# Performance work log

Measured on AMD Instinct MI355X. Metric: run time of the kernel, lower is better.

Reference implementation:

```python
import jax, jax.numpy as jnp
import numpy as np

D_MODEL = 1024
D_STATE = 128
D_CONV = 4
EXPAND = 2
HEADDIM = 64
D_INNER = EXPAND * D_MODEL            # 2048
NHEADS = D_INNER // HEADDIM           # 32
D_IN_PROJ = 2 * D_INNER + 2 * D_STATE + NHEADS  # z, xBC, dt
CONV_DIM = D_INNER + 2 * D_STATE      # depthwise-conv channels


def setup_inputs() -> dict:
    key = jax.random.key(0)
    ks = jax.random.split(key, 8)
    B, L = 2, 2048
    s = lambda k, shape, sc=0.02: jax.random.normal(k, shape, jnp.float32) * sc
    return dict(
        x=jax.random.normal(ks[0], (B, L, D_MODEL), jnp.float32),
        norm1_w=jnp.ones((D_MODEL,), jnp.float32),
        in_proj_w=s(ks[1], (D_IN_PROJ, D_MODEL)),
        conv_w=s(ks[2], (CONV_DIM, D_CONV), 0.2),
        conv_b=jnp.zeros((CONV_DIM,), jnp.float32),
        dt_bias=jnp.log(jnp.expm1(jax.random.uniform(ks[3], (NHEADS,), jnp.float32, 0.001, 0.1))),
        A_log=jnp.log(jax.random.uniform(ks[4], (NHEADS,), jnp.float32, 1.0, 16.0)),
        D=jnp.ones((NHEADS,), jnp.float32),
        mnorm_w=jnp.ones((D_INNER,), jnp.float32),
        out_proj_w=s(ks[5], (D_MODEL, D_INNER)),
        norm2_w=jnp.ones((D_MODEL,), jnp.float32),
        mlp_w1=s(ks[6], (4 * D_MODEL, D_MODEL)),
        mlp_b1=jnp.zeros((4 * D_MODEL,), jnp.float32),
        mlp_w2=s(ks[7], (D_MODEL, 4 * D_MODEL)),
        mlp_b2=jnp.zeros((D_MODEL,), jnp.float32),
    )


def _block_norm(x, w, eps=1e-6):
    # Faithful to source: rms = sqrt(||x||_2^2 + eps) (their .mean(-1) is over a size-1 dim)
    return w * x / jnp.sqrt(jnp.sum(x * x, axis=-1, keepdims=True) + eps)


def _mamba2(x, in_proj_w, conv_w, conv_b, dt_bias, A_log, D, mnorm_w, out_proj_w):
    b, l, _ = x.shape
    zxbcdt = x @ in_proj_w.T                                   # (b,l,D_IN_PROJ)
    z, xBC, dt_raw = jnp.split(zxbcdt, [D_INNER, D_INNER + CONV_DIM], axis=-1)
    # causal depthwise conv1d + silu over (x,B,C)
    pad = jnp.pad(xBC, ((0, 0), (D_CONV - 1, 0), (0, 0)))
    conv = sum(pad[:, k:k + l, :] * conv_w[None, None, :, k] for k in range(D_CONV)) + conv_b
    xBC = jax.nn.silu(conv)
    xh, Bm, Cm = jnp.split(xBC, [D_INNER, D_INNER + D_STATE], axis=-1)
    xh = xh.reshape(b, l, NHEADS, HEADDIM)
    dt = jax.nn.softplus(dt_raw + dt_bias)                     # (b,l,h)
    A = -jnp.exp(A_log)                                        # (h,) scalar-A per head

    def step(hs, inp):
        x_t, dt_t, B_t, C_t = inp                              # (b,h,p),(b,h),(b,n),(b,n)
        dA = jnp.exp(dt_t * A)[:, :, None, None]               # (b,h,1,1)
        hs = hs * dA + (dt_t[:, :, None] * x_t)[..., None] * B_t[:, None, None, :]
        y_t = jnp.einsum('bhpn,bn->bhp', hs, C_t)
        return hs, y_t

    hs0 = jnp.zeros((b, NHEADS, HEADDIM, D_STATE), x.dtype)
    _, ys = jax.lax.scan(step, hs0, (xh.transpose(1, 0, 2, 3), dt.transpose(1, 0, 2),
                                     Bm.transpose(1, 0, 2), Cm.transpose(1, 0, 2)))
    y = ys.transpose(1, 0, 2, 3) + D[None, None, :, None] * xh  # D skip
    y = y.reshape(b, l, D_INNER)
    y = y * jax.nn.silu(z)                                      # gated RMSNorm (mamba2 default)
    y = y / jnp.sqrt(jnp.mean(y * y, axis=-1, keepdims=True) + 1e-5) * mnorm_w
    return y @ out_proj_w.T


def reference(x, norm1_w, in_proj_w, conv_w, conv_b, dt_bias, A_log, D, mnorm_w,
              out_proj_w, norm2_w, mlp_w1, mlp_b1, mlp_w2, mlp_b2):
    x = x + _mamba2(_block_norm(x, norm1_w), in_proj_w, conv_w, conv_b,
                    dt_bias, A_log, D, mnorm_w, out_proj_w)
    h = _block_norm(x, norm2_w)
    h = jax.nn.gelu(h @ mlp_w1.T + mlp_b1, approximate=False) @ mlp_w2.T + mlp_b2
    return x + h
```

## Files before the change

### kernel.cpp

```cpp
#include <hip/hip_runtime.h>
#include <hip/hip_bf16.h>
#include <cstdint>

#define L_SEQ   2048
#define BATCH   2
#define ROWS    (BATCH*L_SEQ)
#define DMODEL  1024
#define DINNER  2048
#define DSTATE  128
#define NHEADS  32
#define DIN_PROJ 4384
#define DIN_PAD  4480
#define CONVDIM  2304
#define DMLP    4096
#define CHUNK   64
#define NCHUNK  (L_SEQ/CHUNK)

typedef __attribute__((ext_vector_type(4))) float f32x4;
typedef __attribute__((ext_vector_type(8))) short bf16x8;
typedef __attribute__((ext_vector_type(4))) short bf16x4;
typedef __attribute__((ext_vector_type(2))) short bf16x2;

static __device__ __forceinline__ short f2bf(float f) {
  union { float f; unsigned int i; } v; v.f = f;
  unsigned int r = v.i + 0x7fffu + ((v.i >> 16) & 1u);
  return (short)(r >> 16);
}
static __device__ __forceinline__ float bf2f(short s) {
  union { unsigned int i; float f; } v; v.i = ((unsigned int)(unsigned short)s) << 16;
  return v.f;
}

static __device__ __forceinline__ void gl2lds16(const void* g, void* l) {
  __builtin_amdgcn_global_load_lds((const __attribute__((address_space(1))) void*)g,
                                   (__attribute__((address_space(3))) void*)l, 16, 0, 0);
}

__global__ __launch_bounds__(256) void cvt_kernel(const float* __restrict__ src, short* __restrict__ dst,
                                                  long rows_src, int kshift)
{
  long i = (((long)blockIdx.x) * 256 + threadIdx.x) * 4;
  long r = i >> kshift;
  bf16x4 o;
  if (r < rows_src) {
    f32x4 v = *(const f32x4*)&src[i];
    o[0] = f2bf(v[0]); o[1] = f2bf(v[1]); o[2] = f2bf(v[2]); o[3] = f2bf(v[3]);
  } else {
    o[0] = 0; o[1] = 0; o[2] = 0; o[3] = 0;
  }
  *(bf16x4*)&dst[i] = o;
}

__global__ __launch_bounds__(256) void rmsnorm_l2_kernel(const float* __restrict__ in,
                                                         const float* __restrict__ w,
                                                         short* __restrict__ out)
{
  int row = blockIdx.x, tid = threadIdx.x;
  const float* xr = in + (long)row * DMODEL;
  f32x4 v = *(const f32x4*)&xr[tid * 4];
  float s = v[0]*v[0] + v[1]*v[1] + v[2]*v[2] + v[3]*v[3];
  for (int o = 32; o; o >>= 1) s += __shfl_down(s, o);
  __shared__ float red[4];
  if ((tid & 63) == 0) red[tid >> 6] = s;
  __syncthreads();
  float sc = rsqrtf(red[0] + red[1] + red[2] + red[3] + 1e-6f);
  f32x4 wv = *(const f32x4*)&w[tid * 4];
  bf16x4 o;
  #pragma unroll
  for (int j = 0; j < 4; j++) o[j] = f2bf(v[j] * sc * wv[j]);
  *(bf16x4*)&out[(long)row * DMODEL + tid * 4] = o;
}

template<int EPI, int STG>
__global__ __launch_bounds__(256)
void gemm_bt_kernel(const short* __restrict__ A, const short* __restrict__ W,
                    const float* __restrict__ bias, const float* __restrict__ resid,
                    void* __restrict__ out, int N, int K)
{
  __shared__ short As[STG][128*64];
  __shared__ short Ws[STG][128*64];
  const int tid = threadIdx.x;
  const int lane = tid & 63, wid = tid >> 6;
  const int wm = wid >> 1, wn = wid & 1;
  const long arow0 = (long)blockIdx.x * 128;
  const long wrow0 = (long)blockIdx.y * 128;
  const int srow = tid >> 3;
  const int sslot = (tid & 7) ^ (srow & 7);
  const int sdst = (tid >> 3) * 64 + (tid & 7) * 8;

  f32x4 acc[4][4];
  #pragma unroll
  for (int m = 0; m < 4; m++)
    #pragma unroll
    for (int n = 0; n < 4; n++)
      #pragma unroll
      for (int j = 0; j < 4; j++) acc[m][n][j] = 0.f;

  auto stage = [&](int buf, long kt) {
    #pragma unroll
    for (int i = 0; i < 4; i++)
      gl2lds16(A + (arow0 + i*32 + srow) * (long)K + kt + sslot*8, &As[buf][i*2048 + sdst]);
    #pragma unroll
    for (int i = 0; i < 4; i++)
      gl2lds16(W + (wrow0 + i*32 + srow) * (long)K + kt + sslot*8, &Ws[buf][i*2048 + sdst]);
  };

  const int nt = K >> 6;
  #pragma unroll
  for (int s = 0; s < STG - 1; s++) stage(s, s << 6);

  const int swz = (lane & 7) << 3;
  for (int t = 0; t < nt; t++) {
    if (t + STG - 1 < nt) {
      stage((t + STG - 1) & (STG - 1), (long)(t + STG - 1) << 6);
      asm volatile("s_waitcnt vmcnt(8)"  ::: "memory");
    } else {
      asm volatile("s_waitcnt vmcnt(0)" ::: "memory");
    }
    __builtin_amdgcn_s_barrier();
    __builtin_amdgcn_sched_barrier(0);
    const int cur = t & (STG - 1);
    #pragma unroll
    for (int kk = 0; kk < 64; kk += 32) {
      bf16x8 a[4], b[4];
      const int ko = kk + (lane >> 4) * 8;
      #pragma unroll
      for (int m = 0; m < 4; m++) {
        int row = wm*64 + m*16 + (lane & 15);
        a[m] = *(const bf16x8*)&As[cur][(row*64 + ko) ^ swz];
      }
      #pragma unroll
      for (int n = 0; n < 4; n++) {
        int row = wn*64 + n*16 + (lane & 15);
        b[n] = *(const bf16x8*)&Ws[cur][(row*64 + ko) ^ swz];
      }
      #pragma unroll
      for (int m = 0; m < 4; m++)
        #pragma unroll
        for (int n = 0; n < 4; n++)
          acc[m][n] = __builtin_amdgcn_mfma_f32_16x16x32_bf16(a[m], b[n], acc[m][n], 0, 0, 0);
    }
    asm volatile("s_waitcnt lgkmcnt(0)" ::: "memory");
    __builtin_amdgcn_sched_barrier(0);
    __builtin_amdgcn_s_barrier();
  }

  const int colf = lane & 15, rowf = (lane >> 4) * 4;
  #pragma unroll
  for (int m = 0; m < 4; m++)
    #pragma unroll
    for (int n = 0; n < 4; n++) {
      long col = wrow0 + wn*64 + n*16 + colf;
      #pragma unroll
      for (int j = 0; j < 4; j++) {
        long row = arow0 + wm*64 + m*16 + rowf + j;
        long idx = row * (long)N + col;
        ((short*)out)[idx] = f2bf(acc[m][n][j]);
      }
    }
}

template<int EPI>
__global__ __launch_bounds__(512)
void gemm256_kernel(const short* __restrict__ A, const short* __restrict__ W,
                    const float* __restrict__ bias, void* __restrict__ out, int N, int K)
{
  __shared__ short As[2][2][8192];
  __shared__ short Bs[2][2][8192];
  const int tid = threadIdx.x;
  const int lane = tid & 63, wid = tid >> 6;
  const int wm = wid >> 2, wn = wid & 3;
  const long arow0 = (long)blockIdx.x * 256;
  const long wrow0 = (long)blockIdx.y * 256;
  const int Kslice = K / gridDim.z;
  const long kbase = (long)blockIdx.z * Kslice;
  const int ntiles = Kslice >> 6;

  const int sr0 = tid >> 2, sr1 = sr0 + 128;
  const int ss  = tid & 3;
  const int scb0 = ss ^ ((sr0 >> 1) & 3);
  const int scb1 = ss ^ ((sr1 >> 1) & 3);
  const int sdst0 = tid * 8, sdst1 = tid * 8 + 4096;

  auto stageA = [&](int tau, int kh) {
    long colb = kbase + (long)tau * 64 + kh * 32;
    gl2lds16(A + (arow0 + sr0) * (long)K + colb + scb0 * 8, &As[tau & 1][kh][sdst0]);
    gl2lds16(A + (arow0 + sr1) * (long)K + colb + scb1 * 8, &As[tau & 1][kh][sdst1]);
  };
  auto stageB = [&](int tau, int kh) {
    long colb = kbase + (long)tau * 64 + kh * 32;
    gl2lds16(W + (wrow0 + sr0) * (long)K + colb + scb0 * 8, &Bs[tau & 1][kh][sdst0]);
    gl2lds16(W + (wrow0 + sr1) * (long)K + colb + scb1 * 8, &Bs[tau & 1][kh][sdst1]);
  };

  f32x4 acc[8][4];
  #pragma unroll
  for (int m = 0; m < 8; m++)
    #pragma unroll
    for (int n = 0; n < 4; n++)
      #pragma unroll
      for (int j = 0; j < 4; j++) acc[m][n][j] = 0.f;

  const int li = lane & 15;
  const int rcb = (((lane >> 4) ^ ((li >> 1) & 3))) * 8;

  stageA(0,0); stageB(0,0); stageA(0,1); stageB(0,1); stageA(1,0); stageB(1,0);
  asm volatile("s_waitcnt vmcnt(8)" ::: "memory");
  __builtin_amdgcn_s_barrier();

  bf16x8 a[8];
  auto phase = [&](int g, int kh, int nh) {
    const int buf = g & 1;
    if (nh == 0) {
      #pragma unroll
      for (int m = 0; m < 8; m++)
        a[m] = *(const bf16x8*)&As[buf][kh][(wm*128 + m*16 + li)*32 + rcb];
    }
    bf16x8 b0 = *(const bf16x8*)&Bs[buf][kh][(wn*64 + (nh*2    )*16 + li)*32 + rcb];
    bf16x8 b1 = *(const bf16x8*)&Bs[buf][kh][(wn*64 + (nh*2 + 1)*16 + li)*32 + rcb];
    if (kh == 0) {
      if (g + 1 < ntiles) { if (nh == 0) stageA(g+1, 1); else stageB(g+1, 1); }
    } else {
      if (g + 2 < ntiles) { if (nh == 0) stageA(g+2, 0); else stageB(g+2, 0); }
    }
    __builtin_amdgcn_s_barrier();
    asm volatile("s_waitcnt lgkmcnt(0)" ::: "memory");
    __builtin_amdgcn_sched_barrier(0);
    __builtin_amdgcn_s_setprio(1);
    #pragma unroll
    for (int m = 0; m < 8; m++) {
      acc[m][nh*2    ] = __builtin_amdgcn_mfma_f32_16x16x32_bf16(a[m], b0, acc[m][nh*2    ], 0, 0, 0);
      acc[m][nh*2 + 1] = __builtin_amdgcn_mfma_f32_16x16x32_bf16(a[m], b1, acc[m][nh*2 + 1], 0, 0, 0);
    }
    __builtin_amdgcn_s_setprio(0);
    if (kh == 0 && nh == 1) {
      if (g < ntiles - 1) asm volatile("s_waitcnt vmcnt(8)" ::: "memory");
      else                asm volatile("s_waitcnt vmcnt(0)" ::: "memory");
    } else if (kh == 1 && nh == 1 && g < ntiles - 1) {
      if (g < ntiles - 2) asm volatile("s_waitcnt vmcnt(8)" ::: "memory");
      else                asm volatile("s_waitcnt vmcnt(4)" ::: "memory");
    }
    __builtin_amdgcn_s_barrier();
  };

  for (int g = 0; g < ntiles; ++g) {
    phase(g, 0, 0); phase(g, 0, 1); phase(g, 1, 0); phase(g, 1, 1);
  }

  const int colf = lane & 15, rowf = (lane >> 4) * 4;
  const long MN = (long)gridDim.x * 256 * N;
  const long po = (long)blockIdx.z * MN;
  #pragma unroll
  for (int m = 0; m < 8; m++)
    #pragma unroll
    for (int n = 0; n < 4; n++) {
      long col = wrow0 + wn*64 + n*16 + colf;
      #pragma unroll
      for (int j = 0; j < 4; j++) {
        long row = arow0 + wm*128 + m*16 + rowf + j;
        long idx = row * (long)N + col;
        float v = acc[m][n][j];
        if (EPI == 2) {
          float t = v + bias[col];
          float ge = 0.5f * t * (1.f + erff(t * 0.70710678118654752f));
          ((short*)out)[idx] = f2bf(ge);
        } else {
          ((short*)out)[po + idx] = f2bf(v);
        }
      }
    }
}

template<bool BIAS>
__global__ __launch_bounds__(256) void reduce_split4_kernel(
    const short* __restrict__ part, const float* __restrict__ resid,
    const float* __restrict__ bias, float* __restrict__ out)
{
  long i = ((long)blockIdx.x * 256 + threadIdx.x) * 8;
  const long MN = (long)ROWS * DMODEL;
  bf16x8 p0 = *(const bf16x8*)&part[i];
  bf16x8 p1 = *(const bf16x8*)&part[i + MN];
  bf16x8 p2 = *(const bf16x8*)&part[i + 2*MN];
  bf16x8 p3 = *(const bf16x8*)&part[i + 3*MN];
  f32x4 r0 = *(const f32x4*)&resid[i];
  f32x4 r1 = *(const f32x4*)&resid[i + 4];
  f32x4 o0, o1;
  #pragma unroll
  for (int j = 0; j < 8; j++) {
    float s = (bf2f(p0[j]) + bf2f(p1[j])) + (bf2f(p2[j]) + bf2f(p3[j]));
    s += (j < 4) ? r0[j] : r1[j - 4];
    if (j < 4) o0[j] = s; else o1[j - 4] = s;
  }
  if (BIAS) {
    int c = (int)(i & (DMODEL - 1));
    f32x4 b0 = *(const f32x4*)&bias[c];
    f32x4 b1 = *(const f32x4*)&bias[c + 4];
    #pragma unroll
    for (int j = 0; j < 4; j++) { o0[j] += b0[j]; o1[j] += b1[j]; }
  }
  *(f32x4*)&out[i] = o0;
  *(f32x4*)&out[i + 4] = o1;
}

__global__ __launch_bounds__(256) void conv_dt_kernel(
    const short* __restrict__ zx, const float* __restrict__ cw, const float* __restrict__ cb,
    const float* __restrict__ dt_bias,
    short* __restrict__ xh, short* __restrict__ Bo, short* __restrict__ Co, float* __restrict__ dto)
{
  const int r0 = blockIdx.x * 8;
  const int tid = threadIdx.x;
  const bool interior = (r0 & (L_SEQ - 1)) != 0;

  auto conv8 = [&](int c0, auto&& emit) {
    const long col = DINNER + c0;
    f32x4 w[8]; float cbv[8];
    #pragma unroll
    for (int j = 0; j < 8; j++) { w[j] = *(const f32x4*)&cw[(c0 + j) * 4]; cbv[j] = cb[c0 + j]; }
    bf16x8 win[11];
    #pragma unroll
    for (int j = 0; j < 3; j++) {
      bf16x8 z;
      #pragma unroll
      for (int q = 0; q < 8; q++) z[q] = 0;
      win[j] = interior ? *(const bf16x8*)&zx[(long)(r0 - 3 + j) * DIN_PAD + col] : z;
    }
    #pragma unroll
    for (int j = 3; j < 11; j++)
      win[j] = *(const bf16x8*)&zx[(long)(r0 - 3 + j) * DIN_PAD + col];
    #pragma unroll
    for (int i = 0; i < 8; i++) {
      float a[8];
      #pragma unroll
      for (int j = 0; j < 8; j++) a[j] = cbv[j];
      #pragma unroll
      for (int k = 0; k < 4; k++)
        #pragma unroll
        for (int j = 0; j < 8; j++) a[j] = fmaf(bf2f(win[i + k][j]), w[j][k], a[j]);
      bf16x8 o;
      #pragma unroll
      for (int j = 0; j < 8; j++) { float s = a[j] / (1.f + __expf(-a[j])); o[j] = f2bf(s); }
      emit(i, o);
    }
  };

  {
    int c0 = tid * 8;
    conv8(c0, [&](int i, bf16x8 o) {
      *(bf16x8*)&xh[(long)(r0 + i) * DINNER + c0] = o;
    });
  }
  if (tid < 32) {
    int c0 = 2048 + tid * 8;
    conv8(c0, [&](int i, bf16x8 o) {
      if (c0 < 2048 + DSTATE) *(bf16x8*)&Bo[(long)(r0 + i) * DSTATE + (c0 - 2048)] = o;
      else                    *(bf16x8*)&Co[(long)(r0 + i) * DSTATE + (c0 - 2048 - DSTATE)] = o;
    });
  } else if (tid < 36) {
    int h0 = (tid - 32) * 8;
    float db[8];
    #pragma unroll
    for (int j = 0; j < 8; j++) db[j] = dt_bias[h0 + j];
    #pragma unroll
    for (int i = 0; i < 8; i++) {
      bf16x8 v = *(const bf16x8*)&zx[(long)(r0 + i) * DIN_PAD + (DINNER + CONVDIM) + h0];
      f32x4 o0, o1;
      #pragma unroll
      for (int j = 0; j < 8; j++) {
        float t = bf2f(v[j]) + db[j];
        float sp = (t > 20.f) ? t : log1pf(__expf(t));
        if (j < 4) o0[j] = sp; else o1[j - 4] = sp;
      }
      *(f32x4*)&dto[(long)(r0 + i) * NHEADS + h0] = o0;
      *(f32x4*)&dto[(long)(r0 + i) * NHEADS + h0 + 4] = o1;
    }
  }
}


__global__ __launch_bounds__(256) void ssd_states_kernel(
    const short* __restrict__ xh, const short* __restrict__ Bm,
    const float* __restrict__ dtb, const float* __restrict__ A_log,
    float* __restrict__ CS, short* __restrict__ SC)
{
  int bid = blockIdx.x;
  int c = bid & 31, h = (bid >> 5) & 31, b = bid >> 10;
  long r0 = (long)b * L_SEQ + c * CHUNK;
  __shared__ short XT[64*72];
  __shared__ short BwT[128*72];
  __shared__ float ws[64];
  int tid = threadIdx.x;

  if (tid < 64) {
    float dtv = dtb[(r0 + tid)*NHEADS + h];
    float A = -__expf(A_log[h]);
    float v = dtv * A;
    #pragma unroll
    for (int o = 1; o < 64; o <<= 1) { float u = __shfl_up(v, o); if (tid >= o) v += u; }
    CS[(long)bid * 64 + tid] = v;
    float cs63 = __shfl(v, 63);
    ws[tid] = __expf(cs63 - v) * dtv;
  }
  #pragma unroll
  for (int i = 0; i < 2; i++) {
    int e = tid + i*256, tau = e & 63, p0 = (e >> 6) * 8;
    bf16x8 v = *(const bf16x8*)&xh[(r0 + tau)*DINNER + h*64 + p0];
    #pragma unroll
    for (int j = 0; j < 8; j++) XT[(p0 + j)*72 + tau] = v[j];
  }
  __syncthreads();
  #pragma unroll
  for (int i = 0; i < 4; i++) {
    int e = tid + i*256, tau = e & 63, n0 = (e >> 6) * 8;
    float w = ws[tau];
    bf16x8 v = *(const bf16x8*)&Bm[(r0 + tau)*DSTATE + n0];
    #pragma unroll
    for (int j = 0; j < 8; j++) BwT[(n0 + j)*72 + tau] = f2bf(bf2f(v[j]) * w);
  }
  __syncthreads();

  int lane = tid & 63, w = tid >> 6;
  f32x4 acc[8];
  #pragma unroll
  for (int nt = 0; nt < 8; nt++) { acc[nt][0]=0.f; acc[nt][1]=0.f; acc[nt][2]=0.f; acc[nt][3]=0.f; }
  #pragma unroll
  for (int kk = 0; kk < 64; kk += 32) {
    int ko = kk + (lane >> 4) * 8;
    bf16x8 a = *(const bf16x8*)&XT[(w*16 + (lane & 15))*72 + ko];
    #pragma unroll
    for (int nt = 0; nt < 8; nt++) {
      bf16x8 bfr = *(const bf16x8*)&BwT[(nt*16 + (lane & 15))*72 + ko];
      acc[nt] = __builtin_amdgcn_mfma_f32_16x16x32_bf16(a, bfr, acc[nt], 0, 0, 0);
    }
  }
  int colf = lane & 15, rowf = (lane >> 4) * 4;
  long sbase = (long)bid * 8192;
  #pragma unroll
  for (int nt = 0; nt < 8; nt++)
    #pragma unroll
    for (int j = 0; j < 4; j++)
      SC[sbase + (w*16 + rowf + j)*128 + nt*16 + colf] = f2bf(acc[nt][j]);
}

__global__ __launch_bounds__(256) void ssd_prefix_kernel(
    const short* __restrict__ SC, const float* __restrict__ CS, short* __restrict__ HP)
{
  int bid = blockIdx.x;
  int q = bid & 3, bh = bid >> 2;
  int tid = threadIdx.x;
  int p = q*16 + (tid >> 4);
  int n0 = (tid & 15) * 8;
  long base = (long)bh * NCHUNK * 8192 + (long)p*128 + n0;
  float H[8];
  #pragma unroll
  for (int j = 0; j < 8; j++) H[j] = 0.f;
  for (int c = 0; c < NCHUNK; c++) {
    long idx = base + (long)c * 8192;
    bf16x8 sc = *(const bf16x8*)&SC[idx];
    bf16x8 hv;
    #pragma unroll
    for (int j = 0; j < 8; j++) hv[j] = f2bf(H[j]);
    *(bf16x8*)&HP[idx] = hv;
    float r = __expf(CS[((long)bh * NCHUNK + c)*64 + 63]);
    #pragma unroll
    for (int j = 0; j < 8; j++) H[j] = H[j]*r + bf2f(sc[j]);
  }
}

__global__ __launch_bounds__(256) void ssd_out_kernel(
    const short* __restrict__ xh, const short* __restrict__ Bm, const short* __restrict__ Cm,
    const float* __restrict__ dtb, const float* __restrict__ CS,
    const short* __restrict__ HP, const float* __restrict__ Dvec,
    short* __restrict__ y)
{
  int bid = blockIdx.x;
  int c = bid & 31, h = (bid >> 5) & 31, b = bid >> 10;
  long r0 = (long)b * L_SEQ + c * CHUNK;
  __shared__ short Csh[64*136];
  __shared__ short Bsh[64*136];
  __shared__ short Ms[64*72];
  __shared__ short XT[64*72];
  __shared__ float csd[64], dts[64];
  int tid = threadIdx.x;

  if (tid < 64) {
    csd[tid] = CS[(long)bid*64 + tid];
    dts[tid] = dtb[(r0 + tid)*NHEADS + h];
  }
  #pragma unroll
  for (int i = 0; i < 4; i++) {
    int e = tid + i*256, tau = e >> 4, n0 = (e & 15) * 8;
    *(bf16x8*)&Bsh[tau*136 + n0] = *(const bf16x8*)&Bm[(r0 + tau)*DSTATE + n0];
    *(bf16x8*)&Csh[tau*136 + n0] = *(const bf16x8*)&Cm[(r0 + tau)*DSTATE + n0];
  }
  #pragma unroll
  for (int i = 0; i < 2; i++) {
    int e = tid + i*256, tau = e & 63, p0 = (e >> 6) * 8;
    bf16x8 v = *(const bf16x8*)&xh[(r0 + tau)*DINNER + h*64 + p0];
    #pragma unroll
    for (int j = 0; j < 8; j++) XT[(p0 + j)*72 + tau] = v[j];
  }
  __syncthreads();

  int lane = tid & 63, w = tid >> 6;
  int colf = lane & 15, rowf = (lane >> 4) * 4;

  f32x4 g[4];
  #pragma unroll
  for (int tt = 0; tt < 4; tt++) { g[tt][0]=0.f; g[tt][1]=0.f; g[tt][2]=0.f; g[tt][3]=0.f; }
  #pragma unroll
  for (int kk = 0; kk < 128; kk += 32) {
    int ko = kk + (lane >> 4) * 8;
    bf16x8 a = *(const bf16x8*)&Csh[(w*16 + (lane & 15))*136 + ko];
    #pragma unroll
    for (int tt = 0; tt < 4; tt++) {
      bf16x8 bfr = *(const bf16x8*)&Bsh[(tt*16 + (lane & 15))*136 + ko];
      g[tt] = __builtin_amdgcn_mfma_f32_16x16x32_bf16(a, bfr, g[tt], 0, 0, 0);
    }
  }
  #pragma unroll
  for (int tt = 0; tt < 4; tt++)
    #pragma unroll
    for (int j = 0; j < 4; j++) {
      int trow = w*16 + rowf + j;
      int tcol = tt*16 + colf;
      float m = (tcol <= trow) ? __expf(csd[trow] - csd[tcol]) * dts[tcol] * g[tt][j] : 0.f;
      Ms[trow*72 + tcol] = f2bf(m);
    }
  __syncthreads();

  f32x4 yv[4], yi[4];
  #pragma unroll
  for (int pt = 0; pt < 4; pt++) {
    yv[pt][0]=0.f; yv[pt][1]=0.f; yv[pt][2]=0.f; yv[pt][3]=0.f;
    yi[pt][0]=0.f; yi[pt][1]=0.f; yi[pt][2]=0.f; yi[pt][3]=0.f;
  }
  #pragma unroll
  for (int kk = 0; kk < 64; kk += 32) {
    int ko = kk + (lane >> 4) * 8;
    bf16x8 a = *(const bf16x8*)&Ms[(w*16 + (lane & 15))*72 + ko];
    #pragma unroll
    for (int pt = 0; pt < 4; pt++) {
      bf16x8 bfr = *(const bf16x8*)&XT[(pt*16 + (lane & 15))*72 + ko];
      yv[pt] = __builtin_amdgcn_mfma_f32_16x16x32_bf16(a, bfr, yv[pt], 0, 0, 0);
    }
  }
  long hpb = (long)bid * 8192;
  #pragma unroll
  for (int kk = 0; kk < 128; kk += 32) {
    int ko = kk + (lane >> 4) * 8;
    bf16x8 a = *(const bf16x8*)&Csh[(w*16 + (lane & 15))*136 + ko];
    #pragma unroll
    for (int pt = 0; pt < 4; pt++) {
      bf16x8 bfr = *(const bf16x8*)&HP[hpb + (long)(pt*16 + (lane & 15))*128 + ko];
      yi[pt] = __builtin_amdgcn_mfma_f32_16x16x32_bf16(a, bfr, yi[pt], 0, 0, 0);
    }
  }
  float Dh = Dvec[h];
  #pragma unroll
  for (int pt = 0; pt < 4; pt++)
    #pragma unroll
    for (int j = 0; j < 4; j++) {
      int trow = w*16 + rowf + j;
      int pcol = pt*16 + colf;
      float sc_ = __expf(csd[trow]);
      float xv = bf2f(XT[pcol*72 + trow]);
      y[(r0 + trow)*DINNER + h*64 + pcol] = f2bf(yv[pt][j] + sc_*yi[pt][j] + Dh*xv);
    }
}

__global__ __launch_bounds__(256) void gate_mnorm_kernel(
    const short* __restrict__ y, const short* __restrict__ zx, const float* __restrict__ mw,
    short* __restrict__ out)
{
  int row = blockIdx.x, tid = threadIdx.x;
  int c0 = tid * 8;
  bf16x8 yv = *(const bf16x8*)&y[(long)row*DINNER + c0];
  bf16x8 zv = *(const bf16x8*)&zx[(long)row*DIN_PAD + c0];
  float g[8]; float ssum = 0.f;
  #pragma unroll
  for (int j = 0; j < 8; j++) {
    float z = bf2f(zv[j]);
    float v = bf2f(yv[j]) * (z / (1.f + __expf(-z)));
    g[j] = v; ssum += v * v;
  }
  for (int o = 32; o; o >>= 1) ssum += __shfl_down(ssum, o);
  __shared__ float red[4];
  if ((tid & 63) == 0) red[tid >> 6] = ssum;
  __syncthreads();
  float tot = red[0] + red[1] + red[2] + red[3];
  float sc = rsqrtf(tot * (1.0f / DINNER) + 1e-5f);
  bf16x8 o;
  #pragma unroll
  for (int j = 0; j < 8; j++) o[j] = f2bf(g[j] * sc * mw[c0 + j]);
  *(bf16x8*)&out[(long)row*DINNER + c0] = o;
}

extern "C" void kernel_launch(void* const* d_in, const int* in_sizes, int n_in,
                              void* d_out, int out_size, void* d_ws, size_t ws_size,
                              hipStream_t stream)
{
  const float* x        = (const float*)d_in[0];
  const float* norm1_w  = (const float*)d_in[1];
  const float* in_proj  = (const float*)d_in[2];
  const float* conv_w   = (const float*)d_in[3];
  const float* conv_b   = (const float*)d_in[4];
  const float* dt_bias  = (const float*)d_in[5];
  const float* A_log    = (const float*)d_in[6];
  const float* Dvec     = (const float*)d_in[7];
  const float* mnorm_w  = (const float*)d_in[8];
  const float* out_proj = (const float*)d_in[9];
  const float* norm2_w  = (const float*)d_in[10];
  const float* mlp_w1   = (const float*)d_in[11];
  const float* mlp_b1   = (const float*)d_in[12];
  const float* mlp_w2   = (const float*)d_in[13];
  const float* mlp_b2   = (const float*)d_in[14];
  float* outp = (float*)d_out;

  uint8_t* wsp = (uint8_t*)d_ws;
  auto take = [&](size_t bytes) { void* p = wsp; wsp += (bytes + 255) & ~(size_t)255; return p; };
  short* W1B  = (short*)take((size_t)DIN_PAD * DMODEL * 2);
  short* W2B  = (short*)take((size_t)DMODEL * DINNER * 2);
  short* W3B  = (short*)take((size_t)DMLP * DMODEL * 2);
  short* W4B  = (short*)take((size_t)DMODEL * DMLP * 2);
  short* X1B  = (short*)take((size_t)ROWS * DMODEL * 2);
  short* ZX   = (short*)take((size_t)ROWS * DIN_PAD * 2);
  short* XH   = (short*)take((size_t)ROWS * DINNER * 2);
  short* BMb  = (short*)take((size_t)ROWS * DSTATE * 2);
  short* CMb  = (short*)take((size_t)ROWS * DSTATE * 2);
  float* DTb  = (float*)take((size_t)ROWS * NHEADS * 4);
  short* Yb   = (short*)take((size_t)ROWS * DINNER * 2);
  short* YGB  = (short*)take((size_t)ROWS * DINNER * 2);
  float* X2   = (float*)take((size_t)ROWS * DMODEL * 4);
  short* X2NB = (short*)take((size_t)ROWS * DMODEL * 2);
  short* H1B  = (short*)take((size_t)ROWS * DMLP * 2);

  short* SC = H1B;
  short* HP = YGB;
  float* CS = (float*)X2NB;
  short* PART = ZX;

  cvt_kernel<<<4480, 256, 0, stream>>>(in_proj, W1B, DIN_PROJ, 10);
  cvt_kernel<<<2048, 256, 0, stream>>>(out_proj, W2B, DMODEL, 11);
  cvt_kernel<<<4096, 256, 0, stream>>>(mlp_w1, W3B, DMLP, 10);
  cvt_kernel<<<4096, 256, 0, stream>>>(mlp_w2, W4B, DMODEL, 12);

  rmsnorm_l2_kernel<<<ROWS, 256, 0, stream>>>(x, norm1_w, X1B);
  gemm_bt_kernel<0,2><<<dim3(ROWS/128, DIN_PAD/128), 256, 0, stream>>>(X1B, W1B, nullptr, nullptr, ZX, DIN_PAD, DMODEL);
  conv_dt_kernel<<<ROWS/8, 256, 0, stream>>>(ZX, conv_w, conv_b, dt_bias, XH, BMb, CMb, DTb);
  ssd_states_kernel<<<BATCH*NHEADS*NCHUNK, 256, 0, stream>>>(XH, BMb, DTb, A_log, CS, SC);
  ssd_prefix_kernel<<<BATCH*NHEADS*4, 256, 0, stream>>>(SC, CS, HP);
  ssd_out_kernel<<<BATCH*NHEADS*NCHUNK, 256, 0, stream>>>(XH, BMb, CMb, DTb, CS, HP, Dvec, Yb);
  gate_mnorm_kernel<<<ROWS, 256, 0, stream>>>(Yb, ZX, mnorm_w, YGB);
  gemm256_kernel<4><<<dim3(16, 4, 4), 512, 0, stream>>>(YGB, W2B, nullptr, PART, DMODEL, DINNER);
  reduce_split4_kernel<false><<<2048, 256, 0, stream>>>(PART, x, nullptr, X2);
  rmsnorm_l2_kernel<<<ROWS, 256, 0, stream>>>(X2, norm2_w, X2NB);
  gemm256_kernel<2><<<dim3(16, 16, 1), 512, 0, stream>>>(X2NB, W3B, mlp_b1, H1B, DMLP, DMODEL);
  gemm256_kernel<4><<<dim3(16, 4, 4), 512, 0, stream>>>(H1B, W4B, nullptr, PART, DMODEL, DMLP);
  reduce_split4_kernel<true><<<2048, 256, 0, stream>>>(PART, X2, mlp_b2, outp);
}
```

Measured before the change: 338.4 us.

## Fuse weight conversions, reduce+norm, and route in_proj through 256-tile GEMM

Merges the four weight-conversion launches into one kernel and fuses the split-K reduction with the second block norm, which removes a launch and a full re-read of the residual stream. The in_proj GEMM moves from the 128-tile kernel to the 256-tile kernel, with DIN_PAD padded to 4608 so it divides evenly. That padding adds some wasted columns. The 256-tile inner loop is also reordered to split its work by M halves instead of N halves, which changes register pressure and fragment reuse.

```diff
diff --git a/kernel.cpp b/kernel.cpp
--- a/kernel.cpp
+++ b/kernel.cpp
@@ -10,7 +10,7 @@
 #define DSTATE  128
 #define NHEADS  32
 #define DIN_PROJ 4384
-#define DIN_PAD  4480
+#define DIN_PAD  4608
 #define CONVDIM  2304
 #define DMLP    4096
 #define CHUNK   64
@@ -36,10 +36,19 @@
                                    (__attribute__((address_space(3))) void*)l, 16, 0, 0);
 }
 
-__global__ __launch_bounds__(256) void cvt_kernel(const float* __restrict__ src, short* __restrict__ dst,
-                                                  long rows_src, int kshift)
-{
-  long i = (((long)blockIdx.x) * 256 + threadIdx.x) * 4;
+__global__ __launch_bounds__(256) void cvt_all_kernel(
+    const float* __restrict__ w1, const float* __restrict__ w2,
+    const float* __restrict__ w3, const float* __restrict__ w4,
+    short* __restrict__ d1, short* __restrict__ d2,
+    short* __restrict__ d3, short* __restrict__ d4)
+{
+  int b = blockIdx.x;
+  const float* src; short* dst; long rows_src; int kshift;
+  if (b < 4608)       { src = w1; dst = d1; rows_src = DIN_PROJ; kshift = 10; }
+  else if (b < 6656)  { src = w2; dst = d2; rows_src = DMODEL;   kshift = 11; b -= 4608; }
+  else if (b < 10752) { src = w3; dst = d3; rows_src = DMLP;     kshift = 10; b -= 6656; }
+  else                { src = w4; dst = d4; rows_src = DMODEL;   kshift = 12; b -= 10752; }
+  long i = ((long)b * 256 + threadIdx.x) * 4;
   long r = i >> kshift;
   bf16x4 o;
   if (r < rows_src) {
@@ -71,93 +80,36 @@
   *(bf16x4*)&out[(long)row * DMODEL + tid * 4] = o;
 }
 
-template<int EPI, int STG>
-__global__ __launch_bounds__(256)
-void gemm_bt_kernel(const short* __restrict__ A, const short* __restrict__ W,
-                    const float* __restrict__ bias, const float* __restrict__ resid,
-                    void* __restrict__ out, int N, int K)
-{
-  __shared__ short As[STG][128*64];
-  __shared__ short Ws[STG][128*64];
-  const int tid = threadIdx.x;
-  const int lane = tid & 63, wid = tid >> 6;
-  const int wm = wid >> 1, wn = wid & 1;
-  const long arow0 = (long)blockIdx.x * 128;
-  const long wrow0 = (long)blockIdx.y * 128;
-  const int srow = tid >> 3;
-  const int sslot = (tid & 7) ^ (srow & 7);
-  const int sdst = (tid >> 3) * 64 + (tid & 7) * 8;
-
-  f32x4 acc[4][4];
-  #pragma unroll
-  for (int m = 0; m < 4; m++)
-    #pragma unroll
-    for (int n = 0; n < 4; n++)
-      #pragma unroll
-      for (int j = 0; j < 4; j++) acc[m][n][j] = 0.f;
-
-  auto stage = [&](int buf, long kt) {
-    #pragma unroll
-    for (int i = 0; i < 4; i++)
-      gl2lds16(A + (arow0 + i*32 + srow) * (long)K + kt + sslot*8, &As[buf][i*2048 + sdst]);
-    #pragma unroll
-    for (int i = 0; i < 4; i++)
-      gl2lds16(W + (wrow0 + i*32 + srow) * (long)K + kt + sslot*8, &Ws[buf][i*2048 + sdst]);
-  };
-
-  const int nt = K >> 6;
-  #pragma unroll
-  for (int s = 0; s < STG - 1; s++) stage(s, s << 6);
-
-  const int swz = (lane & 7) << 3;
-  for (int t = 0; t < nt; t++) {
-    if (t + STG - 1 < nt) {
-      stage((t + STG - 1) & (STG - 1), (long)(t + STG - 1) << 6);
-      asm volatile("s_waitcnt vmcnt(8)"  ::: "memory");
-    } else {
-      asm volatile("s_waitcnt vmcnt(0)" ::: "memory");
-    }
-    __builtin_amdgcn_s_barrier();
-    __builtin_amdgcn_sched_barrier(0);
-    const int cur = t & (STG - 1);
-    #pragma unroll
-    for (int kk = 0; kk < 64; kk += 32) {
-      bf16x8 a[4], b[4];
-      const int ko = kk + (lane >> 4) * 8;
-      #pragma unroll
-      for (int m = 0; m < 4; m++) {
-        int row = wm*64 + m*16 + (lane & 15);
-        a[m] = *(const bf16x8*)&As[cur][(row*64 + ko) ^ swz];
-      }
-      #pragma unroll
-      for (int n = 0; n < 4; n++) {
-        int row = wn*64 + n*16 + (lane & 15);
-        b[n] = *(const bf16x8*)&Ws[cur][(row*64 + ko) ^ swz];
-      }
-      #pragma unroll
-      for (int m = 0; m < 4; m++)
-        #pragma unroll
-        for (int n = 0; n < 4; n++)
-          acc[m][n] = __builtin_amdgcn_mfma_f32_16x16x32_bf16(a[m], b[n], acc[m][n], 0, 0, 0);
-    }
-    asm volatile("s_waitcnt lgkmcnt(0)" ::: "memory");
-    __builtin_amdgcn_sched_barrier(0);
-    __builtin_amdgcn_s_barrier();
-  }
-
-  const int colf = lane & 15, rowf = (lane >> 4) * 4;
-  #pragma unroll
-  for (int m = 0; m < 4; m++)
-    #pragma unroll
-    for (int n = 0; n < 4; n++) {
-      long col = wrow0 + wn*64 + n*16 + colf;
-      #pragma unroll
-      for (int j = 0; j < 4; j++) {
-        long row = arow0 + wm*64 + m*16 + rowf + j;
-        long idx = row * (long)N + col;
-        ((short*)out)[idx] = f2bf(acc[m][n][j]);
-      }
-    }
+__global__ __launch_bounds__(256) void reduce_norm_kernel(
+    const short* __restrict__ part, const float* __restrict__ resid,
+    const float* __restrict__ w, float* __restrict__ X2, short* __restrict__ out)
+{
+  int row = blockIdx.x, tid = threadIdx.x;
+  long i = (long)row * DMODEL + tid * 4;
+  const long MN = (long)ROWS * DMODEL;
+  bf16x4 p0 = *(const bf16x4*)&part[i];
+  bf16x4 p1 = *(const bf16x4*)&part[i + MN];
+  bf16x4 p2 = *(const bf16x4*)&part[i + 2*MN];
+  bf16x4 p3 = *(const bf16x4*)&part[i + 3*MN];
+  f32x4 r = *(const f32x4*)&resid[i];
+  f32x4 v;
+  float s = 0.f;
+  #pragma unroll
+  for (int j = 0; j < 4; j++) {
+    v[j] = (bf2f(p0[j]) + bf2f(p1[j])) + (bf2f(p2[j]) + bf2f(p3[j])) + r[j];
+    s += v[j] * v[j];
+  }
+  *(f32x4*)&X2[i] = v;
+  for (int o = 32; o; o >>= 1) s += __shfl_down(s, o);
+  __shared__ float red[4];
+  if ((tid & 63) == 0) red[tid >> 6] = s;
+  __syncthreads();
+  float sc = rsqrtf(red[0] + red[1] + red[2] + red[3] + 1e-6f);
+  f32x4 wv = *(const f32x4*)&w[tid * 4];
+  bf16x4 o;
+  #pragma unroll
+  for (int j = 0; j < 4; j++) o[j] = f2bf(v[j] * sc * wv[j]);
+  *(bf16x4*)&out[i] = o;
 }
 
 template<int EPI>
@@ -208,35 +160,48 @@
   asm volatile("s_waitcnt vmcnt(8)" ::: "memory");
   __builtin_amdgcn_s_barrier();
 
-  bf16x8 a[8];
-  auto phase = [&](int g, int kh, int nh) {
+  bf16x8 aL[4], aH[4], bfr[4];
+  auto phase = [&](int g, int kh, int mh) {
     const int buf = g & 1;
-    if (nh == 0) {
-      #pragma unroll
-      for (int m = 0; m < 8; m++)
-        a[m] = *(const bf16x8*)&As[buf][kh][(wm*128 + m*16 + li)*32 + rcb];
-    }
-    bf16x8 b0 = *(const bf16x8*)&Bs[buf][kh][(wn*64 + (nh*2    )*16 + li)*32 + rcb];
-    bf16x8 b1 = *(const bf16x8*)&Bs[buf][kh][(wn*64 + (nh*2 + 1)*16 + li)*32 + rcb];
+    if (mh == 0) {
+      #pragma unroll
+      for (int m = 0; m < 4; m++)
+        aL[m] = *(const bf16x8*)&As[buf][kh][(wm*128 + m*16 + li)*32 + rcb];
+      #pragma unroll
+      for (int n = 0; n < 4; n++)
+        bfr[n] = *(const bf16x8*)&Bs[buf][kh][(wn*64 + n*16 + li)*32 + rcb];
+    } else {
+      #pragma unroll
+      for (int m = 0; m < 4; m++)
+        aH[m] = *(const bf16x8*)&As[buf][kh][(wm*128 + (m + 4)*16 + li)*32 + rcb];
+    }
     if (kh == 0) {
-      if (g + 1 < ntiles) { if (nh == 0) stageA(g+1, 1); else stageB(g+1, 1); }
+      if (g + 1 < ntiles) { if (mh == 0) stageA(g+1, 1); else stageB(g+1, 1); }
     } else {
-      if (g + 2 < ntiles) { if (nh == 0) stageA(g+2, 0); else stageB(g+2, 0); }
+      if (g + 2 < ntiles) { if (mh == 0) stageA(g+2, 0); else stageB(g+2, 0); }
     }
     __builtin_amdgcn_s_barrier();
     asm volatile("s_waitcnt lgkmcnt(0)" ::: "memory");
     __builtin_amdgcn_sched_barrier(0);
     __builtin_amdgcn_s_setprio(1);
-    #pragma unroll
-    for (int m = 0; m < 8; m++) {
-      acc[m][nh*2    ] = __builtin_amdgcn_mfma_f32_16x16x32_bf16(a[m], b0, acc[m][nh*2    ], 0, 0, 0);
-      acc[m][nh*2 + 1] = __builtin_amdgcn_mfma_f32_16x16x32_bf16(a[m], b1, acc[m][nh*2 + 1], 0, 0, 0);
+    if (mh == 0) {
+      #pragma unroll
+      for (int m = 0; m < 4; m++)
+        #pragma unroll
+        for (int n = 0; n < 4; n++)
+          acc[m][n] = __builtin_amdgcn_mfma_f32_16x16x32_bf16(aL[m], bfr[n], acc[m][n], 0, 0, 0);
+    } else {
+      #pragma unroll
+      for (int m = 0; m < 4; m++)
+        #pragma unroll
+        for (int n = 0; n < 4; n++)
+          acc[m + 4][n] = __builtin_amdgcn_mfma_f32_16x16x32_bf16(aH[m], bfr[n], acc[m + 4][n], 0, 0, 0);
     }
     __builtin_amdgcn_s_setprio(0);
-    if (kh == 0 && nh == 1) {
+    if (kh == 0 && mh == 1) {
       if (g < ntiles - 1) asm volatile("s_waitcnt vmcnt(8)" ::: "memory");
       else                asm volatile("s_waitcnt vmcnt(0)" ::: "memory");
-    } else if (kh == 1 && nh == 1 && g < ntiles - 1) {
+    } else if (kh == 1 && mh == 1 && g < ntiles - 1) {
       if (g < ntiles - 2) asm volatile("s_waitcnt vmcnt(8)" ::: "memory");
       else                asm volatile("s_waitcnt vmcnt(4)" ::: "memory");
     }
@@ -260,7 +225,9 @@
         long row = arow0 + wm*128 + m*16 + rowf + j;
         long idx = row * (long)N + col;
         float v = acc[m][n][j];
-        if (EPI == 2) {
+        if (EPI == 0) {
+          ((short*)out)[idx] = f2bf(v);
+        } else if (EPI == 2) {
           float t = v + bias[col];
           float ge = 0.5f * t * (1.f + erff(t * 0.70710678118654752f));
           ((short*)out)[idx] = f2bf(ge);
@@ -271,7 +238,6 @@
     }
 }
 
-template<bool BIAS>
 __global__ __launch_bounds__(256) void reduce_split4_kernel(
     const short* __restrict__ part, const float* __restrict__ resid,
     const float* __restrict__ bias, float* __restrict__ out)
@@ -284,19 +250,14 @@
   bf16x8 p3 = *(const bf16x8*)&part[i + 3*MN];
   f32x4 r0 = *(const f32x4*)&resid[i];
   f32x4 r1 = *(const f32x4*)&resid[i + 4];
+  int c = (int)(i & (DMODEL - 1));
+  f32x4 b0 = *(const f32x4*)&bias[c];
+  f32x4 b1 = *(const f32x4*)&bias[c + 4];
   f32x4 o0, o1;
   #pragma unroll
-  for (int j = 0; j < 8; j++) {
-    float s = (bf2f(p0[j]) + bf2f(p1[j])) + (bf2f(p2[j]) + bf2f(p3[j]));
-    s += (j < 4) ? r0[j] : r1[j - 4];
-    if (j < 4) o0[j] = s; else o1[j - 4] = s;
-  }
-  if (BIAS) {
-    int c = (int)(i & (DMODEL - 1));
-    f32x4 b0 = *(const f32x4*)&bias[c];
-    f32x4 b1 = *(const f32x4*)&bias[c + 4];
-    #pragma unroll
-    for (int j = 0; j < 4; j++) { o0[j] += b0[j]; o1[j] += b1[j]; }
+  for (int j = 0; j < 4; j++) {
+    o0[j] = (bf2f(p0[j]) + bf2f(p1[j])) + (bf2f(p2[j]) + bf2f(p3[j])) + r0[j] + b0[j];
+    o1[j] = (bf2f(p0[j+4]) + bf2f(p1[j+4])) + (bf2f(p2[j+4]) + bf2f(p3[j+4])) + r1[j] + b1[j];
   }
   *(f32x4*)&out[i] = o0;
   *(f32x4*)&out[i + 4] = o1;
@@ -639,22 +600,17 @@
   float* CS = (float*)X2NB;
   short* PART = ZX;
 
-  cvt_kernel<<<4480, 256, 0, stream>>>(in_proj, W1B, DIN_PROJ, 10);
-  cvt_kernel<<<2048, 256, 0, stream>>>(out_proj, W2B, DMODEL, 11);
-  cvt_kernel<<<4096, 256, 0, stream>>>(mlp_w1, W3B, DMLP, 10);
-  cvt_kernel<<<4096, 256, 0, stream>>>(mlp_w2, W4B, DMODEL, 12);
-
+  cvt_all_kernel<<<14848, 256, 0, stream>>>(in_proj, out_proj, mlp_w1, mlp_w2, W1B, W2B, W3B, W4B);
   rmsnorm_l2_kernel<<<ROWS, 256, 0, stream>>>(x, norm1_w, X1B);
-  gemm_bt_kernel<0,2><<<dim3(ROWS/128, DIN_PAD/128), 256, 0, stream>>>(X1B, W1B, nullptr, nullptr, ZX, DIN_PAD, DMODEL);
+  gemm256_kernel<0><<<dim3(ROWS/256, DIN_PAD/256, 1), 512, 0, stream>>>(X1B, W1B, nullptr, ZX, DIN_PAD, DMODEL);
   conv_dt_kernel<<<ROWS/8, 256, 0, stream>>>(ZX, conv_w, conv_b, dt_bias, XH, BMb, CMb, DTb);
   ssd_states_kernel<<<BATCH*NHEADS*NCHUNK, 256, 0, stream>>>(XH, BMb, DTb, A_log, CS, SC);
   ssd_prefix_kernel<<<BATCH*NHEADS*4, 256, 0, stream>>>(SC, CS, HP);
   ssd_out_kernel<<<BATCH*NHEADS*NCHUNK, 256, 0, stream>>>(XH, BMb, CMb, DTb, CS, HP, Dvec, Yb);
   gate_mnorm_kernel<<<ROWS, 256, 0, stream>>>(Yb, ZX, mnorm_w, YGB);
   gemm256_kernel<4><<<dim3(16, 4, 4), 512, 0, stream>>>(YGB, W2B, nullptr, PART, DMODEL, DINNER);
-  reduce_split4_kernel<false><<<2048, 256, 0, stream>>>(PART, x, nullptr, X2);
-  rmsnorm_l2_kernel<<<ROWS, 256, 0, stream>>>(X2, norm2_w, X2NB);
+  reduce_norm_kernel<<<ROWS, 256, 0, stream>>>(PART, x, norm2_w, X2, X2NB);
   gemm256_kernel<2><<<dim3(16, 16, 1), 512, 0, stream>>>(X2NB, W3B, mlp_b1, H1B, DMLP, DMODEL);
   gemm256_kernel<4><<<dim3(16, 4, 4), 512, 0, stream>>>(H1B, W4B, nullptr, PART, DMODEL, DMLP);
-  reduce_split4_kernel<true><<<2048, 256, 0, stream>>>(PART, X2, mlp_b2, outp);
-}
+  reduce_split4_kernel<<<2048, 256, 0, stream>>>(PART, X2, mlp_b2, outp);
+}
```

Measured after the change: 339.4 us. No clear change (+0.3%).
